# Performance work log

Hardware: AMD Instinct MI355X
Metric: run time of the kernel (lower is better)

The kernel has to match this reference:

```python
import jax, jax.numpy as jnp
import numpy as np

N_NODES = 32
N_HEADS = 4
HEAD_DIM = 64
NEG_SLOPE = 0.2  # PyG GATConv default LeakyReLU slope


def setup_inputs() -> dict:
    key = jax.random.key(0)
    ks = jax.random.split(key, 8)
    roi_feats = jax.random.normal(ks[0], (N_NODES, 256, 96, 96), dtype=jnp.float32)
    edge_index = jax.random.randint(ks[1], (2, 512), 0, N_NODES, dtype=jnp.int32)
    W = jax.random.normal(ks[2], (256, N_HEADS * HEAD_DIM), dtype=jnp.float32) * 0.0625
    a_src = jax.random.normal(ks[3], (N_HEADS, HEAD_DIM), dtype=jnp.float32) * 0.125
    a_dst = jax.random.normal(ks[4], (N_HEADS, HEAD_DIM), dtype=jnp.float32) * 0.125
    gat_bias = jnp.zeros((N_HEADS * HEAD_DIM,), dtype=jnp.float32)
    cls_W = jax.random.normal(ks[5], (256, 32), dtype=jnp.float32) * 0.0625
    cls_b = jnp.zeros((32,), dtype=jnp.float32)
    return {"roi_feats": roi_feats, "edge_index": edge_index, "W": W,
            "a_src": a_src, "a_dst": a_dst, "gat_bias": gat_bias,
            "cls_W": cls_W, "cls_b": cls_b}


def _gat_conv(x, edge_index, W, a_src, a_dst, bias):
    # x: [N, C]; edge_index: [2, E] (src row 0, dst row 1)
    N = x.shape[0]
    # PyG GATConv adds self-loops by default
    loops = jnp.arange(N, dtype=edge_index.dtype)
    src = jnp.concatenate([edge_index[0], loops])
    dst = jnp.concatenate([edge_index[1], loops])
    h = (x @ W).reshape(N, N_HEADS, HEAD_DIM)          # [N, H, F]
    alpha_s = jnp.einsum('nhf,hf->nh', h, a_src)       # [N, H]
    alpha_d = jnp.einsum('nhf,hf->nh', h, a_dst)
    e = alpha_s[src] + alpha_d[dst]                    # [E', H]
    e = jnp.where(e >= 0, e, NEG_SLOPE * e)            # LeakyReLU
    # segment softmax over incoming edges of each dst node
    m = jax.ops.segment_max(e, dst, num_segments=N)    # [N, H]
    ex = jnp.exp(e - m[dst])
    denom = jax.ops.segment_sum(ex, dst, num_segments=N)
    alpha = ex / denom[dst]                            # [E', H]
    out = jax.ops.segment_sum(alpha[:, :, None] * h[src], dst, num_segments=N)
    return out.reshape(N, N_HEADS * HEAD_DIM) + bias


def reference(roi_feats, edge_index, W, a_src, a_dst, gat_bias, cls_W, cls_b):
    # [N, C, H, W] -> [N, C] spatial mean pool
    x = roi_feats.mean(axis=(2, 3))
    x = _gat_conv(x, edge_index, W, a_src, a_dst, gat_bias)
    logit = jax.nn.silu(x) @ cls_W + cls_b             # [N, num_au]
    return logit
```

## Files before the change

### kernel.cpp

```cpp
#include <hip/hip_runtime.h>
#include <math.h>

#define N_NODES  32
#define N_HEADS  4
#define HEAD_DIM 64
#define CDIM     256
#define HWPIX    9216
#define ROWF4    2304
#define E_BASE   512
#define E_TOT    544
#define NEG_SLOPE 0.2f
#define XS       257

__global__ __launch_bounds__(256, 4) void pool_kernel(const float* __restrict__ roi,
                                                      float* __restrict__ x) {
    const int wave = threadIdx.x >> 6, lane = threadIdx.x & 63;
    const int row = blockIdx.x * 4 + wave;
    const float4* p = reinterpret_cast<const float4*>(roi) + (size_t)row * ROWF4 + lane;

    float4 A[12], B[12];
    float s = 0.f;

#pragma unroll
    for (int j = 0; j < 12; ++j) A[j] = p[j * 64];
#pragma unroll
    for (int j = 0; j < 12; ++j) B[j] = p[(12 + j) * 64];
#pragma unroll
    for (int j = 0; j < 12; ++j) s += (A[j].x + A[j].y) + (A[j].z + A[j].w);
#pragma unroll
    for (int j = 0; j < 12; ++j) A[j] = p[(24 + j) * 64];
#pragma unroll
    for (int j = 0; j < 12; ++j) s += (B[j].x + B[j].y) + (B[j].z + B[j].w);
#pragma unroll
    for (int j = 0; j < 12; ++j) s += (A[j].x + A[j].y) + (A[j].z + A[j].w);

#pragma unroll
    for (int off = 32; off; off >>= 1) s += __shfl_down(s, off);
    if (lane == 0) x[row] = s * (1.0f / (float)HWPIX);
}

__global__ __launch_bounds__(256) void gat_kernel(const int* __restrict__ edge_index,
                                                  const float* __restrict__ x,
                                                  const float* __restrict__ W,
                                                  const float* __restrict__ a_src,
                                                  const float* __restrict__ a_dst,
                                                  const float* __restrict__ gat_bias,
                                                  const float* __restrict__ cls_W,
                                                  const float* __restrict__ cls_b,
                                                  float* __restrict__ out) {
    const int n = blockIdx.x;
    const int t = threadIdx.x;

    __shared__ float    xs[N_NODES * XS];
    __shared__ __align__(16) float asl[CDIM];
    __shared__ __align__(16) float adl[CDIM];
    __shared__ float    was[CDIM * N_HEADS];
    __shared__ float    wad[CDIM * N_HEADS];
    __shared__ float    als[N_NODES * N_HEADS];
    __shared__ float    adn[N_HEADS];
    __shared__ unsigned msegu[N_HEADS];
    __shared__ float    dseg[N_HEADS];
    __shared__ float    M[N_NODES * N_HEADS];
    __shared__ float    y[N_HEADS * CDIM];
    __shared__ float    sv[CDIM];
    __shared__ float    red[8][32];

    asl[t] = a_src[t];
    adl[t] = a_dst[t];
    if (t < N_HEADS) { msegu[t] = 0u; dseg[t] = 0.f; }
    if (t < N_NODES * N_HEADS) M[t] = 0.f;
    __syncthreads();

#pragma unroll
    for (int k = 0; k < 8; ++k) {
        const int i4 = t + k * 256;
        const float4 v = ((const float4*)x)[i4];
        const int i = i4 * 4, s = i >> 8, c = i & 255;
        xs[s * XS + c + 0] = v.x;
        xs[s * XS + c + 1] = v.y;
        xs[s * XS + c + 2] = v.z;
        xs[s * XS + c + 3] = v.w;
    }

    {
        float accs[N_HEADS] = {0.f, 0.f, 0.f, 0.f};
        float accd[N_HEADS] = {0.f, 0.f, 0.f, 0.f};
        const float4* wr  = (const float4*)(W + t * CDIM);
        const float4* as4 = (const float4*)asl;
        const float4* ad4 = (const float4*)adl;
#pragma unroll 16
        for (int q = 0; q < 64; ++q) {
            const float4 w = wr[q], av = as4[q], dv = ad4[q];
            const int hd = q >> 4;
            accs[hd] += w.x * av.x + w.y * av.y + w.z * av.z + w.w * av.w;
            accd[hd] += w.x * dv.x + w.y * dv.y + w.z * dv.z + w.w * dv.w;
        }
#pragma unroll
        for (int hd = 0; hd < N_HEADS; ++hd) {
            was[t * N_HEADS + hd] = accs[hd];
            wad[t * N_HEADS + hd] = accd[hd];
        }
    }
    __syncthreads();

    if (t < 132) {
        if (t < 128) {
            const int s = t >> 2, hd = t & 3;
            const float* xrow = &xs[s * XS];
            float acc = 0.f;
#pragma unroll 8
            for (int c = 0; c < CDIM; ++c) acc += xrow[c] * was[c * N_HEADS + hd];
            als[t] = acc;
        } else {
            const int hd = t - 128;
            const float* xrow = &xs[n * XS];
            float acc = 0.f;
#pragma unroll 8
            for (int c = 0; c < CDIM; ++c) acc += xrow[c] * wad[c * N_HEADS + hd];
            adn[hd] = acc;
        }
    }
    __syncthreads();

    for (int e = t; e < E_TOT; e += 256) {
        int s0, d;
        if (e < E_BASE) { s0 = edge_index[e]; d = edge_index[E_BASE + e]; }
        else            { s0 = e - E_BASE;    d = s0; }
        if (d == n) {
#pragma unroll
            for (int hd = 0; hd < N_HEADS; ++hd) {
                float v = als[s0 * N_HEADS + hd] + adn[hd];
                v = (v >= 0.f) ? v : NEG_SLOPE * v;
                const int iv = __float_as_int(v);
                const unsigned key = (iv < 0) ? ~(unsigned)iv
                                              : ((unsigned)iv | 0x80000000u);
                atomicMax(&msegu[hd], key);
            }
        }
    }
    __syncthreads();

    float mx[N_HEADS];
#pragma unroll
    for (int hd = 0; hd < N_HEADS; ++hd) {
        const unsigned key = msegu[hd];
        const int im = (key & 0x80000000u) ? (int)(key & 0x7fffffffu) : (int)~key;
        mx[hd] = __int_as_float(im);
    }

    for (int e = t; e < E_TOT; e += 256) {
        int s0, d;
        if (e < E_BASE) { s0 = edge_index[e]; d = edge_index[E_BASE + e]; }
        else            { s0 = e - E_BASE;    d = s0; }
        if (d == n) {
#pragma unroll
            for (int hd = 0; hd < N_HEADS; ++hd) {
                float v = als[s0 * N_HEADS + hd] + adn[hd];
                v = (v >= 0.f) ? v : NEG_SLOPE * v;
                const float ex = expf(v - mx[hd]);
                atomicAdd(&dseg[hd], ex);
                atomicAdd(&M[s0 * N_HEADS + hd], ex);
            }
        }
    }
    __syncthreads();

    if (t < N_NODES * N_HEADS) M[t] /= dseg[t & 3];
    __syncthreads();

    {
        const int hd = t >> 6, l = t & 63;
        float acc0 = 0.f, acc1 = 0.f, acc2 = 0.f, acc3 = 0.f;
#pragma unroll
        for (int s = 0; s < N_NODES; ++s) {
            const float m = M[s * N_HEADS + hd];
            const float* xrow = &xs[s * XS + l];
            acc0 += m * xrow[0];
            acc1 += m * xrow[64];
            acc2 += m * xrow[128];
            acc3 += m * xrow[192];
        }
        y[hd * CDIM + l]       = acc0;
        y[hd * CDIM + l + 64]  = acc1;
        y[hd * CDIM + l + 128] = acc2;
        y[hd * CDIM + l + 192] = acc3;
    }
    __syncthreads();

    {
        const int head = t >> 6;
        const float* yrow = &y[head * CDIM];
        float acc = 0.f;
#pragma unroll 16
        for (int c = 0; c < CDIM; ++c) acc += yrow[c] * W[c * CDIM + t];
        const float v = acc + gat_bias[t];
        sv[t] = v / (1.0f + expf(-v));
    }
    __syncthreads();

    {
        const int j = t & 31, g = t >> 5;
        float a = 0.f;
#pragma unroll
        for (int c0 = 0; c0 < 32; ++c0) {
            const int c = g * 32 + c0;
            a += sv[c] * cls_W[c * 32 + j];
        }
        red[g][j] = a;
    }
    __syncthreads();
    if (t < 32) {
        float s2 = cls_b[t];
#pragma unroll
        for (int g2 = 0; g2 < 8; ++g2) s2 += red[g2][t];
        out[n * 32 + t] = s2;
    }
}

extern "C" void kernel_launch(void* const* d_in, const int* in_sizes, int n_in,
                              void* d_out, int out_size, void* d_ws, size_t ws_size,
                              hipStream_t stream) {
    const float* roi   = (const float*)d_in[0];
    const int*   eidx  = (const int*)d_in[1];
    const float* W     = (const float*)d_in[2];
    const float* a_src = (const float*)d_in[3];
    const float* a_dst = (const float*)d_in[4];
    const float* gbias = (const float*)d_in[5];
    const float* clsW  = (const float*)d_in[6];
    const float* clsb  = (const float*)d_in[7];
    float* out = (float*)d_out;

    float* x = (float*)d_ws;

    pool_kernel<<<(N_NODES * CDIM) / 4, 256, 0, stream>>>(roi, x);
    gat_kernel<<<N_NODES, 256, 0, stream>>>(eidx, x, W, a_src, a_dst,
                                            gbias, clsW, clsb, out);
}
```

Measured before the change: 72.51 us.

## Fuse pooling and GAT into one kernel with a global atomic-counter barrier

Merges the pooling and GAT kernels into a single launch of 1024 blocks, each pooling two rows per wave. The first 32 blocks then run the GAT stage after spinning on a device-scope atomic counter until every block has finished pooling. To overlap with that wait, the W·a projections and edge-index loads are hoisted ahead of the barrier, and the dst-projection is reduced with wave shuffles instead of a serial loop. This saves a kernel launch gap but adds a memset, a spin-wait, and the risk of deadlock if not all 1024 blocks can be resident at once.

After: 165.6 us. 128% more time.

```diff
diff --git a/kernel.cpp b/kernel.cpp
--- a/kernel.cpp
+++ b/kernel.cpp
@@ -3,7 +3,6 @@
 
 #define N_NODES  32
 #define N_HEADS  4
-#define HEAD_DIM 64
 #define CDIM     256
 #define HWPIX    9216
 #define ROWF4    2304
@@ -11,64 +10,100 @@
 #define E_TOT    544
 #define NEG_SLOPE 0.2f
 #define XS       257
-
-__global__ __launch_bounds__(256, 4) void pool_kernel(const float* __restrict__ roi,
-                                                      float* __restrict__ x) {
-    const int wave = threadIdx.x >> 6, lane = threadIdx.x & 63;
-    const int row = blockIdx.x * 4 + wave;
-    const float4* p = reinterpret_cast<const float4*>(roi) + (size_t)row * ROWF4 + lane;
-
-    float4 A[12], B[12];
-    float s = 0.f;
-
-#pragma unroll
-    for (int j = 0; j < 12; ++j) A[j] = p[j * 64];
-#pragma unroll
-    for (int j = 0; j < 12; ++j) B[j] = p[(12 + j) * 64];
-#pragma unroll
-    for (int j = 0; j < 12; ++j) s += (A[j].x + A[j].y) + (A[j].z + A[j].w);
-#pragma unroll
-    for (int j = 0; j < 12; ++j) A[j] = p[(24 + j) * 64];
-#pragma unroll
-    for (int j = 0; j < 12; ++j) s += (B[j].x + B[j].y) + (B[j].z + B[j].w);
-#pragma unroll
-    for (int j = 0; j < 12; ++j) s += (A[j].x + A[j].y) + (A[j].z + A[j].w);
-
-#pragma unroll
-    for (int off = 32; off; off >>= 1) s += __shfl_down(s, off);
-    if (lane == 0) x[row] = s * (1.0f / (float)HWPIX);
-}
-
-__global__ __launch_bounds__(256) void gat_kernel(const int* __restrict__ edge_index,
-                                                  const float* __restrict__ x,
-                                                  const float* __restrict__ W,
-                                                  const float* __restrict__ a_src,
-                                                  const float* __restrict__ a_dst,
-                                                  const float* __restrict__ gat_bias,
-                                                  const float* __restrict__ cls_W,
-                                                  const float* __restrict__ cls_b,
-                                                  float* __restrict__ out) {
-    const int n = blockIdx.x;
-    const int t = threadIdx.x;
-
+#define GRID     1024
+
+__global__ __launch_bounds__(256, 4) void fused_kernel(
+    const float* __restrict__ roi,
+    const int*   __restrict__ edge_index,
+    const float* __restrict__ W,
+    const float* __restrict__ a_src,
+    const float* __restrict__ a_dst,
+    const float* __restrict__ gat_bias,
+    const float* __restrict__ cls_W,
+    const float* __restrict__ cls_b,
+    float*       __restrict__ x,
+    unsigned*    __restrict__ counter,
+    float*       __restrict__ out)
+{
     __shared__ float    xs[N_NODES * XS];
-    __shared__ __align__(16) float asl[CDIM];
-    __shared__ __align__(16) float adl[CDIM];
-    __shared__ float    was[CDIM * N_HEADS];
-    __shared__ float    wad[CDIM * N_HEADS];
-    __shared__ float    als[N_NODES * N_HEADS];
+    __shared__ float    wasy[N_HEADS * CDIM];
+    __shared__ float    alsM[256];
+    __shared__ float    sv[CDIM];
     __shared__ float    adn[N_HEADS];
     __shared__ unsigned msegu[N_HEADS];
     __shared__ float    dseg[N_HEADS];
-    __shared__ float    M[N_NODES * N_HEADS];
-    __shared__ float    y[N_HEADS * CDIM];
-    __shared__ float    sv[CDIM];
-    __shared__ float    red[8][32];
-
-    asl[t] = a_src[t];
-    adl[t] = a_dst[t];
-    if (t < N_HEADS) { msegu[t] = 0u; dseg[t] = 0.f; }
-    if (t < N_NODES * N_HEADS) M[t] = 0.f;
+    __shared__ float    wscr[16];
+
+    const int t = threadIdx.x;
+    const int wave = t >> 6, lane = t & 63;
+
+#pragma unroll
+    for (int r = 0; r < 2; ++r) {
+        const int row = (blockIdx.x * 4 + wave) * 2 + r;
+        const float4* p = (const float4*)roi + (size_t)row * ROWF4 + lane;
+        float4 A[12], B[12];
+        float s = 0.f;
+#pragma unroll
+        for (int j = 0; j < 12; ++j) A[j] = p[j * 64];
+#pragma unroll
+        for (int j = 0; j < 12; ++j) B[j] = p[(12 + j) * 64];
+#pragma unroll
+        for (int j = 0; j < 12; ++j) s += (A[j].x + A[j].y) + (A[j].z + A[j].w);
+#pragma unroll
+        for (int j = 0; j < 12; ++j) A[j] = p[(24 + j) * 64];
+#pragma unroll
+        for (int j = 0; j < 12; ++j) s += (B[j].x + B[j].y) + (B[j].z + B[j].w);
+#pragma unroll
+        for (int j = 0; j < 12; ++j) s += (A[j].x + A[j].y) + (A[j].z + A[j].w);
+#pragma unroll
+        for (int off = 32; off; off >>= 1) s += __shfl_down(s, off);
+        if (lane == 0) x[row] = s * (1.0f / (float)HWPIX);
+    }
+    __syncthreads();
+    if (t == 0) {
+        __threadfence();
+        __hip_atomic_fetch_add(counter, 1u, __ATOMIC_RELEASE,
+                               __HIP_MEMORY_SCOPE_AGENT);
+    }
+    if (blockIdx.x >= N_NODES) return;
+
+    const int n = blockIdx.x;
+
+    float wadreg[N_HEADS];
+    {
+        float accs[4] = {0.f, 0.f, 0.f, 0.f};
+        float accd[4] = {0.f, 0.f, 0.f, 0.f};
+        const float4* wr  = (const float4*)(W + t * CDIM);
+        const float4* as4 = (const float4*)a_src;
+        const float4* ad4 = (const float4*)a_dst;
+#pragma unroll 16
+        for (int q = 0; q < 64; ++q) {
+            const float4 w = wr[q], av = as4[q], dv = ad4[q];
+            const int hd = q >> 4;
+            accs[hd] += w.x*av.x + w.y*av.y + w.z*av.z + w.w*av.w;
+            accd[hd] += w.x*dv.x + w.y*dv.y + w.z*dv.z + w.w*dv.w;
+        }
+#pragma unroll
+        for (int hd = 0; hd < 4; ++hd) {
+            wasy[t * 4 + hd] = accs[hd];
+            wadreg[hd] = accd[hd];
+        }
+    }
+
+    int es[3], ed[3];
+    es[0] = edge_index[t];        ed[0] = edge_index[E_BASE + t];
+    es[1] = edge_index[t + 256];  ed[1] = edge_index[E_BASE + t + 256];
+    es[2] = t;                    ed[2] = (t < E_TOT - E_BASE) ? t : -1;
+
+    if (t < 128) alsM[128 + t] = 0.f;
+    if (t < 4)   { msegu[t] = 0u; dseg[t] = 0.f; }
+
+    if (t == 0) {
+        while (__hip_atomic_load(counter, __ATOMIC_RELAXED,
+                                 __HIP_MEMORY_SCOPE_AGENT) < GRID)
+            __builtin_amdgcn_s_sleep(2);
+        __threadfence();
+    }
     __syncthreads();
 
 #pragma unroll
@@ -81,55 +116,41 @@
         xs[s * XS + c + 2] = v.z;
         xs[s * XS + c + 3] = v.w;
     }
-
-    {
-        float accs[N_HEADS] = {0.f, 0.f, 0.f, 0.f};
-        float accd[N_HEADS] = {0.f, 0.f, 0.f, 0.f};
-        const float4* wr  = (const float4*)(W + t * CDIM);
-        const float4* as4 = (const float4*)asl;
-        const float4* ad4 = (const float4*)adl;
-#pragma unroll 16
-        for (int q = 0; q < 64; ++q) {
-            const float4 w = wr[q], av = as4[q], dv = ad4[q];
-            const int hd = q >> 4;
-            accs[hd] += w.x * av.x + w.y * av.y + w.z * av.z + w.w * av.w;
-            accd[hd] += w.x * dv.x + w.y * dv.y + w.z * dv.z + w.w * dv.w;
-        }
-#pragma unroll
-        for (int hd = 0; hd < N_HEADS; ++hd) {
-            was[t * N_HEADS + hd] = accs[hd];
-            wad[t * N_HEADS + hd] = accd[hd];
-        }
-    }
-    __syncthreads();
-
-    if (t < 132) {
-        if (t < 128) {
-            const int s = t >> 2, hd = t & 3;
-            const float* xrow = &xs[s * XS];
-            float acc = 0.f;
+    __syncthreads();
+
+    {
+        const float xv = xs[n * XS + t];
+        float p0 = xv * wadreg[0], p1 = xv * wadreg[1];
+        float p2 = xv * wadreg[2], p3 = xv * wadreg[3];
+#pragma unroll
+        for (int off = 32; off; off >>= 1) {
+            p0 += __shfl_down(p0, off); p1 += __shfl_down(p1, off);
+            p2 += __shfl_down(p2, off); p3 += __shfl_down(p3, off);
+        }
+        if (lane == 0) {
+            wscr[wave * 4 + 0] = p0; wscr[wave * 4 + 1] = p1;
+            wscr[wave * 4 + 2] = p2; wscr[wave * 4 + 3] = p3;
+        }
+    }
+    __syncthreads();
+    if (t < 4) adn[t] = wscr[t] + wscr[4 + t] + wscr[8 + t] + wscr[12 + t];
+
+    if (t < 128) {
+        const int s = t >> 2, hd = t & 3;
+        const float* xrow = &xs[s * XS];
+        float acc = 0.f;
 #pragma unroll 8
-            for (int c = 0; c < CDIM; ++c) acc += xrow[c] * was[c * N_HEADS + hd];
-            als[t] = acc;
-        } else {
-            const int hd = t - 128;
-            const float* xrow = &xs[n * XS];
-            float acc = 0.f;
-#pragma unroll 8
-            for (int c = 0; c < CDIM; ++c) acc += xrow[c] * wad[c * N_HEADS + hd];
-            adn[hd] = acc;
-        }
-    }
-    __syncthreads();
-
-    for (int e = t; e < E_TOT; e += 256) {
-        int s0, d;
-        if (e < E_BASE) { s0 = edge_index[e]; d = edge_index[E_BASE + e]; }
-        else            { s0 = e - E_BASE;    d = s0; }
-        if (d == n) {
-#pragma unroll
-            for (int hd = 0; hd < N_HEADS; ++hd) {
-                float v = als[s0 * N_HEADS + hd] + adn[hd];
+        for (int c = 0; c < CDIM; ++c) acc += xrow[c] * wasy[c * 4 + hd];
+        alsM[t] = acc;
+    }
+    __syncthreads();
+
+#pragma unroll
+    for (int k = 0; k < 3; ++k) {
+        if (ed[k] == n) {
+#pragma unroll
+            for (int hd = 0; hd < 4; ++hd) {
+                float v = alsM[es[k] * 4 + hd] + adn[hd];
                 v = (v >= 0.f) ? v : NEG_SLOPE * v;
                 const int iv = __float_as_int(v);
                 const unsigned key = (iv < 0) ? ~(unsigned)iv
@@ -140,56 +161,51 @@
     }
     __syncthreads();
 
-    float mx[N_HEADS];
-#pragma unroll
-    for (int hd = 0; hd < N_HEADS; ++hd) {
+    float mx[4];
+#pragma unroll
+    for (int hd = 0; hd < 4; ++hd) {
         const unsigned key = msegu[hd];
         const int im = (key & 0x80000000u) ? (int)(key & 0x7fffffffu) : (int)~key;
         mx[hd] = __int_as_float(im);
     }
 
-    for (int e = t; e < E_TOT; e += 256) {
-        int s0, d;
-        if (e < E_BASE) { s0 = edge_index[e]; d = edge_index[E_BASE + e]; }
-        else            { s0 = e - E_BASE;    d = s0; }
-        if (d == n) {
-#pragma unroll
-            for (int hd = 0; hd < N_HEADS; ++hd) {
-                float v = als[s0 * N_HEADS + hd] + adn[hd];
+#pragma unroll
+    for (int k = 0; k < 3; ++k) {
+        if (ed[k] == n) {
+#pragma unroll
+            for (int hd = 0; hd < 4; ++hd) {
+                float v = alsM[es[k] * 4 + hd] + adn[hd];
                 v = (v >= 0.f) ? v : NEG_SLOPE * v;
                 const float ex = expf(v - mx[hd]);
                 atomicAdd(&dseg[hd], ex);
-                atomicAdd(&M[s0 * N_HEADS + hd], ex);
+                atomicAdd(&alsM[128 + es[k] * 4 + hd], ex);
             }
         }
     }
     __syncthreads();
-
-    if (t < N_NODES * N_HEADS) M[t] /= dseg[t & 3];
-    __syncthreads();
-
-    {
-        const int hd = t >> 6, l = t & 63;
-        float acc0 = 0.f, acc1 = 0.f, acc2 = 0.f, acc3 = 0.f;
+    if (t < 128) alsM[128 + t] /= dseg[t & 3];
+    __syncthreads();
+
+    {
+        const int hd = t >> 6;
+        float a0 = 0.f, a1 = 0.f, a2 = 0.f, a3 = 0.f;
 #pragma unroll
         for (int s = 0; s < N_NODES; ++s) {
-            const float m = M[s * N_HEADS + hd];
-            const float* xrow = &xs[s * XS + l];
-            acc0 += m * xrow[0];
-            acc1 += m * xrow[64];
-            acc2 += m * xrow[128];
-            acc3 += m * xrow[192];
-        }
-        y[hd * CDIM + l]       = acc0;
-        y[hd * CDIM + l + 64]  = acc1;
-        y[hd * CDIM + l + 128] = acc2;
-        y[hd * CDIM + l + 192] = acc3;
-    }
-    __syncthreads();
-
-    {
-        const int head = t >> 6;
-        const float* yrow = &y[head * CDIM];
+            const float m = alsM[128 + s * 4 + hd];
+            const float* xrow = &xs[s * XS + lane];
+            a0 += m * xrow[0];   a1 += m * xrow[64];
+            a2 += m * xrow[128]; a3 += m * xrow[192];
+        }
+        wasy[hd * CDIM + lane]       = a0;
+        wasy[hd * CDIM + lane + 64]  = a1;
+        wasy[hd * CDIM + lane + 128] = a2;
+        wasy[hd * CDIM + lane + 192] = a3;
+    }
+    __syncthreads();
+
+    {
+        const int hd = t >> 6;
+        const float* yrow = &wasy[hd * CDIM];
         float acc = 0.f;
 #pragma unroll 16
         for (int c = 0; c < CDIM; ++c) acc += yrow[c] * W[c * CDIM + t];
@@ -206,13 +222,13 @@
             const int c = g * 32 + c0;
             a += sv[c] * cls_W[c * 32 + j];
         }
-        red[g][j] = a;
+        alsM[g * 32 + j] = a;
     }
     __syncthreads();
     if (t < 32) {
         float s2 = cls_b[t];
 #pragma unroll
-        for (int g2 = 0; g2 < 8; ++g2) s2 += red[g2][t];
+        for (int g2 = 0; g2 < 8; ++g2) s2 += alsM[g2 * 32 + t];
         out[n * 32 + t] = s2;
     }
 }
@@ -230,9 +246,10 @@
     const float* clsb  = (const float*)d_in[7];
     float* out = (float*)d_out;
 
-    float* x = (float*)d_ws;
-
-    pool_kernel<<<(N_NODES * CDIM) / 4, 256, 0, stream>>>(roi, x);
-    gat_kernel<<<N_NODES, 256, 0, stream>>>(eidx, x, W, a_src, a_dst,
-                                            gbias, clsW, clsb, out);
+    unsigned* counter = (unsigned*)d_ws;
+    float*    x       = (float*)((char*)d_ws + 256);
+
+    hipMemsetAsync(d_ws, 0, 64, stream);
+    fused_kernel<<<GRID, 256, 0, stream>>>(roi, eidx, W, a_src, a_dst,
+                                           gbias, clsW, clsb, x, counter, out);
 }
```

## Prefetch GAT inputs into registers and vectorize the W projection over waves

Applied to the files above, without the earlier changes.

The GAT kernel now issues its global loads (x, attention vectors, edge indices, biases) up front into registers before the first barrier, so their latencies overlap. The edge loops reuse those preloaded indices, and each thread reduces its edges to one max per head before the atomic, which cuts shared-memory atomics. The final y·W projection is restructured so each wave covers a 64-row slice of W with float4 loads, followed by a cross-wave shared reduction. The costs are higher register pressure and one extra reduction step; the pooling kernel, which dominates runtime, is unchanged.

After: 71.32 us. About the same (-1.6%).

```diff
diff --git a/kernel.cpp b/kernel.cpp
--- a/kernel.cpp
+++ b/kernel.cpp
@@ -50,6 +50,7 @@
                                                   float* __restrict__ out) {
     const int n = blockIdx.x;
     const int t = threadIdx.x;
+    const int wavg = t >> 6, lane = t & 63;
 
     __shared__ float    xs[N_NODES * XS];
     __shared__ __align__(16) float asl[CDIM];
@@ -63,42 +64,51 @@
     __shared__ float    M[N_NODES * N_HEADS];
     __shared__ float    y[N_HEADS * CDIM];
     __shared__ float    sv[CDIM];
-    __shared__ float    red[8][32];
-
-    asl[t] = a_src[t];
-    adl[t] = a_dst[t];
-    if (t < N_HEADS) { msegu[t] = 0u; dseg[t] = 0.f; }
-    if (t < N_NODES * N_HEADS) M[t] = 0.f;
-    __syncthreads();
+    __shared__ float4   red4[N_HEADS][64];
+    __shared__ float    cred[8][32];
+
+    float4 xv[8];
+#pragma unroll
+    for (int k = 0; k < 8; ++k) xv[k] = ((const float4*)x)[t + k * 256];
+    const float asr = a_src[t], adr = a_dst[t];
+    const int es0 = edge_index[t],       ed0 = edge_index[E_BASE + t];
+    const int es1 = edge_index[256 + t], ed1 = edge_index[E_BASE + 256 + t];
+    float4 bias4 = make_float4(0.f, 0.f, 0.f, 0.f);
+    if (t < 64) bias4 = ((const float4*)gat_bias)[t];
+    float cb = 0.f;
+    if (t < 32) cb = cls_b[t];
 
 #pragma unroll
     for (int k = 0; k < 8; ++k) {
-        const int i4 = t + k * 256;
-        const float4 v = ((const float4*)x)[i4];
-        const int i = i4 * 4, s = i >> 8, c = i & 255;
-        xs[s * XS + c + 0] = v.x;
-        xs[s * XS + c + 1] = v.y;
-        xs[s * XS + c + 2] = v.z;
-        xs[s * XS + c + 3] = v.w;
-    }
-
-    {
-        float accs[N_HEADS] = {0.f, 0.f, 0.f, 0.f};
-        float accd[N_HEADS] = {0.f, 0.f, 0.f, 0.f};
-        const float4* wr  = (const float4*)(W + t * CDIM);
+        const int i = (t + k * 256) * 4, s = i >> 8, c = i & 255;
+        xs[s * XS + c + 0] = xv[k].x;
+        xs[s * XS + c + 1] = xv[k].y;
+        xs[s * XS + c + 2] = xv[k].z;
+        xs[s * XS + c + 3] = xv[k].w;
+    }
+    asl[t] = asr;
+    adl[t] = adr;
+    if (t < 128) M[t] = 0.f;
+    if (t < 4) { msegu[t] = 0u; dseg[t] = 0.f; }
+    __syncthreads();
+
+    {
+        float accs[4] = {0.f, 0.f, 0.f, 0.f};
+        float accd[4] = {0.f, 0.f, 0.f, 0.f};
+        const float4* wr  = (const float4*)(W + (size_t)t * CDIM);
         const float4* as4 = (const float4*)asl;
         const float4* ad4 = (const float4*)adl;
-#pragma unroll 16
-        for (int q = 0; q < 64; ++q) {
-            const float4 w = wr[q], av = as4[q], dv = ad4[q];
-            const int hd = q >> 4;
+#pragma unroll 32
+        for (int j = 0; j < 64; ++j) {
+            const float4 w = wr[j], av = as4[j], dv = ad4[j];
+            const int hd = j >> 4;
             accs[hd] += w.x * av.x + w.y * av.y + w.z * av.z + w.w * av.w;
             accd[hd] += w.x * dv.x + w.y * dv.y + w.z * dv.z + w.w * dv.w;
         }
 #pragma unroll
-        for (int hd = 0; hd < N_HEADS; ++hd) {
-            was[t * N_HEADS + hd] = accs[hd];
-            wad[t * N_HEADS + hd] = accd[hd];
+        for (int hd = 0; hd < 4; ++hd) {
+            was[t * 4 + hd] = accs[hd];
+            wad[t * 4 + hd] = accd[hd];
         }
     }
     __syncthreads();
@@ -109,29 +119,38 @@
             const float* xrow = &xs[s * XS];
             float acc = 0.f;
 #pragma unroll 8
-            for (int c = 0; c < CDIM; ++c) acc += xrow[c] * was[c * N_HEADS + hd];
+            for (int c = 0; c < CDIM; ++c) acc += xrow[c] * was[c * 4 + hd];
             als[t] = acc;
         } else {
             const int hd = t - 128;
             const float* xrow = &xs[n * XS];
             float acc = 0.f;
 #pragma unroll 8
-            for (int c = 0; c < CDIM; ++c) acc += xrow[c] * wad[c * N_HEADS + hd];
+            for (int c = 0; c < CDIM; ++c) acc += xrow[c] * wad[c * 4 + hd];
             adn[hd] = acc;
         }
     }
     __syncthreads();
 
-    for (int e = t; e < E_TOT; e += 256) {
-        int s0, d;
-        if (e < E_BASE) { s0 = edge_index[e]; d = edge_index[E_BASE + e]; }
-        else            { s0 = e - E_BASE;    d = s0; }
-        if (d == n) {
-#pragma unroll
-            for (int hd = 0; hd < N_HEADS; ++hd) {
-                float v = als[s0 * N_HEADS + hd] + adn[hd];
-                v = (v >= 0.f) ? v : NEG_SLOPE * v;
-                const int iv = __float_as_int(v);
+    {
+        const bool sl = (t < 32) && (t == n);
+#pragma unroll
+        for (int hd = 0; hd < 4; ++hd) {
+            float best = -INFINITY;
+            if (ed0 == n) {
+                float v = als[es0 * 4 + hd] + adn[hd];
+                best = fmaxf(best, (v >= 0.f) ? v : NEG_SLOPE * v);
+            }
+            if (ed1 == n) {
+                float v = als[es1 * 4 + hd] + adn[hd];
+                best = fmaxf(best, (v >= 0.f) ? v : NEG_SLOPE * v);
+            }
+            if (sl) {
+                float v = als[n * 4 + hd] + adn[hd];
+                best = fmaxf(best, (v >= 0.f) ? v : NEG_SLOPE * v);
+            }
+            if (best > -INFINITY) {
+                const int iv = __float_as_int(best);
                 const unsigned key = (iv < 0) ? ~(unsigned)iv
                                               : ((unsigned)iv | 0x80000000u);
                 atomicMax(&msegu[hd], key);
@@ -140,79 +159,106 @@
     }
     __syncthreads();
 
-    float mx[N_HEADS];
-#pragma unroll
-    for (int hd = 0; hd < N_HEADS; ++hd) {
+    float mx[4];
+#pragma unroll
+    for (int hd = 0; hd < 4; ++hd) {
         const unsigned key = msegu[hd];
         const int im = (key & 0x80000000u) ? (int)(key & 0x7fffffffu) : (int)~key;
         mx[hd] = __int_as_float(im);
     }
 
-    for (int e = t; e < E_TOT; e += 256) {
-        int s0, d;
-        if (e < E_BASE) { s0 = edge_index[e]; d = edge_index[E_BASE + e]; }
-        else            { s0 = e - E_BASE;    d = s0; }
-        if (d == n) {
-#pragma unroll
-            for (int hd = 0; hd < N_HEADS; ++hd) {
-                float v = als[s0 * N_HEADS + hd] + adn[hd];
+    {
+        const bool sl = (t < 32) && (t == n);
+#pragma unroll
+        for (int hd = 0; hd < 4; ++hd) {
+            if (ed0 == n) {
+                float v = als[es0 * 4 + hd] + adn[hd];
                 v = (v >= 0.f) ? v : NEG_SLOPE * v;
                 const float ex = expf(v - mx[hd]);
                 atomicAdd(&dseg[hd], ex);
-                atomicAdd(&M[s0 * N_HEADS + hd], ex);
-            }
-        }
-    }
-    __syncthreads();
-
-    if (t < N_NODES * N_HEADS) M[t] /= dseg[t & 3];
-    __syncthreads();
-
-    {
-        const int hd = t >> 6, l = t & 63;
-        float acc0 = 0.f, acc1 = 0.f, acc2 = 0.f, acc3 = 0.f;
+                atomicAdd(&M[es0 * 4 + hd], ex);
+            }
+            if (ed1 == n) {
+                float v = als[es1 * 4 + hd] + adn[hd];
+                v = (v >= 0.f) ? v : NEG_SLOPE * v;
+                const float ex = expf(v - mx[hd]);
+                atomicAdd(&dseg[hd], ex);
+                atomicAdd(&M[es1 * 4 + hd], ex);
+            }
+            if (sl) {
+                float v = als[n * 4 + hd] + adn[hd];
+                v = (v >= 0.f) ? v : NEG_SLOPE * v;
+                const float ex = expf(v - mx[hd]);
+                atomicAdd(&dseg[hd], ex);
+                atomicAdd(&M[n * 4 + hd], ex);
+            }
+        }
+    }
+    __syncthreads();
+    if (t < 128) M[t] /= dseg[t & 3];
+    __syncthreads();
+
+    {
+        const int hd = wavg;
+        float a0 = 0.f, a1 = 0.f, a2 = 0.f, a3 = 0.f;
 #pragma unroll
         for (int s = 0; s < N_NODES; ++s) {
-            const float m = M[s * N_HEADS + hd];
-            const float* xrow = &xs[s * XS + l];
-            acc0 += m * xrow[0];
-            acc1 += m * xrow[64];
-            acc2 += m * xrow[128];
-            acc3 += m * xrow[192];
-        }
-        y[hd * CDIM + l]       = acc0;
-        y[hd * CDIM + l + 64]  = acc1;
-        y[hd * CDIM + l + 128] = acc2;
-        y[hd * CDIM + l + 192] = acc3;
-    }
-    __syncthreads();
-
-    {
-        const int head = t >> 6;
-        const float* yrow = &y[head * CDIM];
-        float acc = 0.f;
+            const float m = M[s * 4 + hd];
+            const float* xrow = &xs[s * XS + lane];
+            a0 += m * xrow[0];   a1 += m * xrow[64];
+            a2 += m * xrow[128]; a3 += m * xrow[192];
+        }
+        y[hd * CDIM + lane]       = a0;
+        y[hd * CDIM + lane + 64]  = a1;
+        y[hd * CDIM + lane + 128] = a2;
+        y[hd * CDIM + lane + 192] = a3;
+    }
+    __syncthreads();
+
+    {
+        const int hd = lane >> 4;
+        const float* yrow = &y[hd * CDIM];
+        float4 acc = make_float4(0.f, 0.f, 0.f, 0.f);
 #pragma unroll 16
-        for (int c = 0; c < CDIM; ++c) acc += yrow[c] * W[c * CDIM + t];
-        const float v = acc + gat_bias[t];
-        sv[t] = v / (1.0f + expf(-v));
-    }
-    __syncthreads();
-
-    {
-        const int j = t & 31, g = t >> 5;
+        for (int cc = 0; cc < 64; ++cc) {
+            const int c = wavg * 64 + cc;
+            const float4 w4 = ((const float4*)(W + (size_t)c * CDIM))[lane];
+            const float yv = yrow[c];
+            acc.x += yv * w4.x; acc.y += yv * w4.y;
+            acc.z += yv * w4.z; acc.w += yv * w4.w;
+        }
+        red4[wavg][lane] = acc;
+    }
+    __syncthreads();
+    if (t < 64) {
+        const float4 s0 = red4[0][t], s1 = red4[1][t];
+        const float4 s2 = red4[2][t], s3 = red4[3][t];
+        float v0 = s0.x + s1.x + s2.x + s3.x + bias4.x;
+        float v1 = s0.y + s1.y + s2.y + s3.y + bias4.y;
+        float v2 = s0.z + s1.z + s2.z + s3.z + bias4.z;
+        float v3 = s0.w + s1.w + s2.w + s3.w + bias4.w;
+        sv[4 * t + 0] = v0 / (1.0f + expf(-v0));
+        sv[4 * t + 1] = v1 / (1.0f + expf(-v1));
+        sv[4 * t + 2] = v2 / (1.0f + expf(-v2));
+        sv[4 * t + 3] = v3 / (1.0f + expf(-v3));
+    }
+    __syncthreads();
+
+    {
+        const int j = t & 31, g8 = t >> 5;
         float a = 0.f;
 #pragma unroll
         for (int c0 = 0; c0 < 32; ++c0) {
-            const int c = g * 32 + c0;
+            const int c = g8 * 32 + c0;
             a += sv[c] * cls_W[c * 32 + j];
         }
-        red[g][j] = a;
+        cred[g8][j] = a;
     }
     __syncthreads();
     if (t < 32) {
-        float s2 = cls_b[t];
-#pragma unroll
-        for (int g2 = 0; g2 < 8; ++g2) s2 += red[g2][t];
+        float s2 = cb;
+#pragma unroll
+        for (int g2 = 0; g2 < 8; ++g2) s2 += cred[g2][t];
         out[n * 32 + t] = s2;
     }
 }
```
